# Performance work log

Hardware: AMD Instinct MI355X
Metric: run time of the kernel (lower is better)

The kernel has to match this reference:

```python
import jax, jax.numpy as jnp
import numpy as np

EMBED_DIM = 1024
NUM_HEADS = 16
HEAD_DIM = EMBED_DIM // NUM_HEADS
ROPE_BASE = 10000.0


def _rope_cos_sin(seq_len, head_dim, dtype):
    # Standard RoPE (ESM-style rotate_half): freqs outer(t, inv_freq), emb = cat(freqs, freqs)
    inv_freq = 1.0 / (ROPE_BASE ** (jnp.arange(0, head_dim, 2, dtype=jnp.float32) / head_dim))
    t = jnp.arange(seq_len, dtype=jnp.float32)
    freqs = jnp.einsum('s,d->sd', t, inv_freq)          # [s, d/2]
    emb = jnp.concatenate([freqs, freqs], axis=-1)      # [s, d]
    return jnp.cos(emb).astype(dtype), jnp.sin(emb).astype(dtype)


def _rotate_half(x):
    x1, x2 = jnp.split(x, 2, axis=-1)
    return jnp.concatenate([-x2, x1], axis=-1)


def _apply_rope(x, cos, sin):
    # x: [b, h, s, d]; cos/sin: [s, d] broadcast over b, h
    return x * cos + _rotate_half(x) * sin


def setup_inputs() -> dict:
    key = jax.random.key(0)
    ks = jax.random.split(key, 5)
    b, s, e = 4, 2048, EMBED_DIM
    scale = 1.0 / np.sqrt(e)
    x = jax.random.normal(ks[0], (b, s, e), dtype=jnp.float32)
    Wqkv = jax.random.normal(ks[1], (e, 3 * e), dtype=jnp.float32) * scale
    bqkv = jnp.zeros((3 * e,), dtype=jnp.float32)
    Wo = jax.random.normal(ks[2], (e, e), dtype=jnp.float32) * scale
    bo = jnp.zeros((e,), dtype=jnp.float32)
    return {"x": x, "Wqkv": Wqkv, "bqkv": bqkv, "Wo": Wo, "bo": bo}


def reference(x, Wqkv, bqkv, Wo, bo):
    b, s, e = x.shape
    h, d = NUM_HEADS, HEAD_DIM
    qkv = jnp.einsum('bse,ef->bsf', x, Wqkv) + bqkv          # [b, s, 3e]
    q, k, v = jnp.split(qkv, 3, axis=-1)
    # b s (h d) -> b h s d
    q = q.reshape(b, s, h, d).transpose(0, 2, 1, 3)
    k = k.reshape(b, s, h, d).transpose(0, 2, 1, 3)
    v = v.reshape(b, s, h, d).transpose(0, 2, 1, 3)
    cos, sin = _rope_cos_sin(s, d, x.dtype)
    q = _apply_rope(q, cos, sin)
    k = _apply_rope(k, cos, sin)
    # scaled dot product attention (no mask, no dropout, non-causal)
    scores = jnp.einsum('bhqd,bhkd->bhqk', q, k) / jnp.asarray(np.sqrt(d), x.dtype)
    attn = jax.nn.softmax(scores, axis=-1)
    out = jnp.einsum('bhqk,bhkd->bhqd', attn, v)             # [b, h, s, d]
    out = out.transpose(0, 2, 1, 3).reshape(b, s, e)         # b h s d -> b s (h d)
    return jnp.einsum('bse,ef->bsf', out, Wo) + bo
```

## Files before the change

### kernel.cpp

```cpp
#include <hip/hip_runtime.h>
#include <stdint.h>
#include <stddef.h>

typedef __bf16 bf16;
typedef __attribute__((ext_vector_type(8))) __bf16 bf16x8;
typedef __attribute__((ext_vector_type(4))) __bf16 bf16x4;
typedef __attribute__((ext_vector_type(4))) float f32x4;
typedef __attribute__((ext_vector_type(4))) float float4v;

#define BATCH 4
#define SEQ   2048
#define EMB   1024
#define NH    16
#define HD    64
#define F3    3072

#define MFMA16(a, b, c) __builtin_amdgcn_mfma_f32_16x16x32_bf16((a), (b), (c), 0, 0, 0)

__device__ __forceinline__ void gload_lds16(const bf16* g, bf16* l) {
  __builtin_amdgcn_global_load_lds(
      (const __attribute__((address_space(1))) uint32_t*)g,
      (__attribute__((address_space(3))) uint32_t*)l, 16, 0, 0);
}

__device__ __forceinline__ int mod10(int x) { return x >= 10 ? x - 10 : x; }

__global__ __launch_bounds__(256) void rope_table(float* __restrict__ cosT,
                                                  float* __restrict__ sinT) {
  int idx = blockIdx.x * 256 + threadIdx.x;
  int pos = idx >> 5, d1 = idx & 31;
  float inv = powf(10000.0f, -(float)(2 * d1) / 64.0f);
  float th = (float)pos * inv;
  cosT[idx] = cosf(th);
  sinT[idx] = sinf(th);
}

__global__ __launch_bounds__(256) void convert_bf16(const float* __restrict__ src,
                                                    bf16* __restrict__ dst, int n4) {
  int i = blockIdx.x * 256 + threadIdx.x;
  if (i >= n4) return;
  float4v v = ((const float4v*)src)[i];
  bf16x4 o;
#pragma unroll
  for (int k = 0; k < 4; ++k) o[k] = (bf16)v[k];
  ((bf16x4*)dst)[i] = o;
}

__global__ __launch_bounds__(256) void transpose_f32_bf16(const float* __restrict__ in,
                                                          bf16* __restrict__ out,
                                                          int R, int C) {
  __shared__ bf16 tile[32][33];
  const int tx = threadIdx.x & 31;
  const int ty = threadIdx.x >> 5;
  const int c0 = blockIdx.x * 32, r0 = blockIdx.y * 32;
#pragma unroll
  for (int kk = 0; kk < 4; ++kk) {
    int r = ty + kk * 8;
    tile[r][tx] = (bf16)in[(size_t)(r0 + r) * C + c0 + tx];
  }
  __syncthreads();
#pragma unroll
  for (int kk = 0; kk < 4; ++kk) {
    int r = ty + kk * 8;
    out[(size_t)(c0 + r) * R + r0 + tx] = tile[tx][r];
  }
}

__device__ __forceinline__ void gemm256_core(bf16* lds,
                                             const bf16* __restrict__ Abase,
                                             const bf16* __restrict__ Bbase,
                                             f32x4 (&acc)[8][4]) {
  const int tid = threadIdx.x;
  const int w = tid >> 6, lane = tid & 63;
  const int lhi = lane >> 4, llo = lane & 15, l7 = llo & 7;
  const int wr = w >> 2, wc = w & 3;
  const int srow = lane >> 3;
  const int sk16 = (lane & 7) ^ srow;
  const size_t g_lane = (size_t)(w * 16 + srow) * EMB + sk16 * 8;
  bf16* ldsw = lds + w * 1024;

  const int ka0 = (lhi * 8) ^ (l7 << 3);
  const int ka1 = (32 + lhi * 8) ^ (l7 << 3);
  const int arow = llo * 64;
  const int brow = ((wc & 1) * 64 + llo) * 64;

#pragma unroll
  for (int i = 0; i < 8; ++i)
#pragma unroll
    for (int j = 0; j < 4; ++j) acc[i][j] = (f32x4){0.f, 0.f, 0.f, 0.f};

#define STAGE(baseptr, slot)                              \
  do {                                                    \
    const bf16* _b = (baseptr);                           \
    bf16* _l = ldsw + (slot) * 8192;                      \
    gload_lds16(_b + g_lane, _l);                         \
    gload_lds16(_b + g_lane + 8 * EMB, _l + 512);         \
  } while (0)

  STAGE(Abase, 0);
  STAGE(Abase + 128 * EMB, 1);
  STAGE(Bbase, 2);
  STAGE(Bbase + 128 * EMB, 3);
  STAGE(Abase + 64, 4);
  STAGE(Abase + 128 * EMB + 64, 5);
  asm volatile("s_waitcnt vmcnt(4)" ::: "memory");
  __builtin_amdgcn_s_barrier();

  int rs = 0;
#pragma unroll 1
  for (int t = 0; t < 16; ++t) {
    const bf16* ldsA = lds + mod10(rs + wr) * 8192 + arow;
    const bf16* ldsB = lds + mod10(rs + 2 + (wc >> 1)) * 8192 + brow;
    const int k1 = (t + 1) * 64;
    const int k2 = (t + 2) * 64;
    bf16x8 a[4][2], b0[2][2], b1[2][2];

#pragma unroll
    for (int i = 0; i < 4; ++i) {
      a[i][0] = *(const bf16x8*)(ldsA + i * 1024 + ka0);
      a[i][1] = *(const bf16x8*)(ldsA + i * 1024 + ka1);
    }
#pragma unroll
    for (int j = 0; j < 2; ++j) {
      b0[j][0] = *(const bf16x8*)(ldsB + j * 1024 + ka0);
      b0[j][1] = *(const bf16x8*)(ldsB + j * 1024 + ka1);
    }
    if (t < 15) STAGE(Bbase + k1, mod10(rs + 6));
    __builtin_amdgcn_s_barrier();
    asm volatile("s_waitcnt lgkmcnt(0)" ::: "memory");
    __builtin_amdgcn_sched_barrier(0);
    __builtin_amdgcn_s_setprio(1);
#pragma unroll
    for (int i = 0; i < 4; ++i)
#pragma unroll
      for (int j = 0; j < 2; ++j) {
        acc[i][j] = MFMA16(a[i][0], b0[j][0], acc[i][j]);
        acc[i][j] = MFMA16(a[i][1], b0[j][1], acc[i][j]);
      }
    __builtin_amdgcn_s_setprio(0);
    __builtin_amdgcn_s_barrier();

#pragma unroll
    for (int j = 0; j < 2; ++j) {
      b1[j][0] = *(const bf16x8*)(ldsB + 2048 + j * 1024 + ka0);
      b1[j][1] = *(const bf16x8*)(ldsB + 2048 + j * 1024 + ka1);
    }
    if (t < 15) STAGE(Bbase + 128 * EMB + k1, mod10(rs + 7));
    __builtin_amdgcn_s_barrier();
    asm volatile("s_waitcnt lgkmcnt(0)" ::: "memory");
    __builtin_amdgcn_sched_barrier(0);
    __builtin_amdgcn_s_setprio(1);
#pragma unroll
    for (int i = 0; i < 4; ++i)
#pragma unroll
      for (int j = 0; j < 2; ++j) {
        acc[i][2 + j] = MFMA16(a[i][0], b1[j][0], acc[i][2 + j]);
        acc[i][2 + j] = MFMA16(a[i][1], b1[j][1], acc[i][2 + j]);
      }
    __builtin_amdgcn_s_setprio(0);
    __builtin_amdgcn_s_barrier();

#pragma unroll
    for (int i = 0; i < 4; ++i) {
      a[i][0] = *(const bf16x8*)(ldsA + 4096 + i * 1024 + ka0);
      a[i][1] = *(const bf16x8*)(ldsA + 4096 + i * 1024 + ka1);
    }
    if (t < 14) STAGE(Abase + k2, mod10(rs + 8));
    __builtin_amdgcn_s_barrier();
    asm volatile("s_waitcnt lgkmcnt(0)" ::: "memory");
    __builtin_amdgcn_sched_barrier(0);
    __builtin_amdgcn_s_setprio(1);
#pragma unroll
    for (int i = 0; i < 4; ++i)
#pragma unroll
      for (int j = 0; j < 2; ++j) {
        acc[4 + i][2 + j] = MFMA16(a[i][0], b1[j][0], acc[4 + i][2 + j]);
        acc[4 + i][2 + j] = MFMA16(a[i][1], b1[j][1], acc[4 + i][2 + j]);
      }
    __builtin_amdgcn_s_setprio(0);
    __builtin_amdgcn_s_barrier();

    if (t < 14) STAGE(Abase + 128 * EMB + k2, mod10(rs + 9));
    __builtin_amdgcn_s_barrier();
    asm volatile("s_waitcnt lgkmcnt(0)" ::: "memory");
    __builtin_amdgcn_sched_barrier(0);
    __builtin_amdgcn_s_setprio(1);
#pragma unroll
    for (int i = 0; i < 4; ++i)
#pragma unroll
      for (int j = 0; j < 2; ++j) {
        acc[4 + i][j] = MFMA16(a[i][0], b0[j][0], acc[4 + i][j]);
        acc[4 + i][j] = MFMA16(a[i][1], b0[j][1], acc[4 + i][j]);
      }
    __builtin_amdgcn_s_setprio(0);
    if (t < 14) {
      asm volatile("s_waitcnt vmcnt(4)" ::: "memory");
    } else if (t == 14) {
      asm volatile("s_waitcnt vmcnt(0)" ::: "memory");
    }
    if (t < 15) __builtin_amdgcn_s_barrier();

    rs += 4;
    if (rs >= 10) rs -= 10;
  }
#undef STAGE
}

__global__ __launch_bounds__(512, 2) void qkv8_kernel(
    const bf16* __restrict__ x, const bf16* __restrict__ wT,
    const float* __restrict__ bias, bf16* __restrict__ qo, bf16* __restrict__ ko,
    bf16* __restrict__ vo, const float* __restrict__ cosT,
    const float* __restrict__ sinT) {
  extern __shared__ __align__(16) bf16 ldsb[];
  const int orig = blockIdx.x;
  const int wg = (orig & 7) * 48 + (orig >> 3);
  const int bx = wg % 12, by = wg / 12;
  const int row_a0 = by * 256, row_b0 = bx * 256;

  f32x4 acc[8][4];
  gemm256_core(ldsb, x + (size_t)row_a0 * EMB, wT + (size_t)row_b0 * EMB, acc);

  const int tid = threadIdx.x;
  const int w = tid >> 6, lane = tid & 63;
  const int lhi = lane >> 4, llo = lane & 15;
  const int wr = w >> 2, wc = w & 3;

  const int f0 = row_b0 + wc * 64;
  const int part = f0 >> 10;
  const int hh = (f0 & 1023) >> 6;
  const int m_base = row_a0 + wr * 128;

  float bvals[4];
#pragma unroll
  for (int j = 0; j < 4; ++j) bvals[j] = bias[f0 + j * 16 + llo];

  if (part == 2) {
#pragma unroll
    for (int mi = 0; mi < 8; ++mi) {
      int m0 = m_base + mi * 16 + lhi * 4;
      int bb = m0 >> 11, pos0 = m0 & 2047;
#pragma unroll
      for (int j = 0; j < 4; ++j) {
        int dd = j * 16 + llo;
        bf16x4 pk;
#pragma unroll
        for (int r = 0; r < 4; ++r) pk[r] = (bf16)(acc[mi][j][r] + bvals[j]);
        *(bf16x4*)(vo + ((size_t)(bb * NH + hh) * HD + dd) * SEQ + pos0) = pk;
      }
    }
  } else {
    bf16* dst = (part == 0) ? qo : ko;
    const float qs = (part == 0) ? 0.125f : 1.0f;
#pragma unroll
    for (int mi = 0; mi < 8; ++mi) {
#pragma unroll
      for (int r = 0; r < 4; ++r) {
        int m = m_base + mi * 16 + lhi * 4 + r;
        int bb = m >> 11, pos = m & 2047;
        size_t base = ((size_t)(bb * NH + hh) * SEQ + pos) * HD;
#pragma unroll
        for (int j = 0; j < 2; ++j) {
          int d1 = j * 16 + llo;
          float x1 = acc[mi][j][r] + bvals[j];
          float x2 = acc[mi][j + 2][r] + bvals[j + 2];
          float cth = cosT[pos * 32 + d1];
          float sth = sinT[pos * 32 + d1];
          dst[base + d1] = (bf16)((x1 * cth - x2 * sth) * qs);
          dst[base + d1 + 32] = (bf16)((x2 * cth + x1 * sth) * qs);
        }
      }
    }
  }
}

__global__ __launch_bounds__(512, 2) void outproj8_kernel(
    const bf16* __restrict__ a_in, const bf16* __restrict__ wT,
    const float* __restrict__ bo, float* __restrict__ out) {
  extern __shared__ __align__(16) bf16 ldsb[];
  const int orig = blockIdx.x;
  const int wg = (orig & 7) * 16 + (orig >> 3);
  const int bx = wg % 4, by = wg / 4;
  const int row_a0 = by * 256, row_b0 = bx * 256;

  f32x4 acc[8][4];
  gemm256_core(ldsb, a_in + (size_t)row_a0 * EMB, wT + (size_t)row_b0 * EMB, acc);

  const int tid = threadIdx.x;
  const int w = tid >> 6, lane = tid & 63;
  const int lhi = lane >> 4, llo = lane & 15;
  const int wr = w >> 2, wc = w & 3;

  const int col0 = row_b0 + wc * 64;
  const int m_base = row_a0 + wr * 128;
  float bvals[4];
#pragma unroll
  for (int j = 0; j < 4; ++j) bvals[j] = bo[col0 + j * 16 + llo];
#pragma unroll
  for (int mi = 0; mi < 8; ++mi) {
#pragma unroll
    for (int r = 0; r < 4; ++r) {
      int m = m_base + mi * 16 + lhi * 4 + r;
#pragma unroll
      for (int j = 0; j < 4; ++j)
        out[(size_t)m * EMB + col0 + j * 16 + llo] = acc[mi][j][r] + bvals[j];
    }
  }
}

__global__ __launch_bounds__(512) void attn_kernel(const bf16* __restrict__ q,
                                                   const bf16* __restrict__ k,
                                                   const bf16* __restrict__ vT,
                                                   bf16* __restrict__ o) {
  __shared__ __align__(16) bf16 smem[32768];
  bf16* Qs = smem;

  const int tid = threadIdx.x, w = tid >> 6, lane = tid & 63;
  const int lhi = lane >> 4, llo = lane & 15;
  const int l7 = llo & 7;
  const int bidx = blockIdx.x;
  const int vblk = (bidx & 7) * 64 + (bidx >> 3);
  const int qt = vblk & 7, bh = vblk >> 3;
  const bf16* qbase = q + (size_t)bh * SEQ * HD + qt * 256 * HD;
  const bf16* kbase = k + (size_t)bh * SEQ * HD;
  const bf16* vbase = vT + (size_t)bh * HD * SEQ;
  bf16* Pw = smem + w * 2048;

  const int rowc = lane >> 3;
  const int sw8 = (lane & 7) ^ rowc;

#pragma unroll
  for (int c = 0; c < 4; ++c) {
    int chunk = w * 4 + c;
    int row = chunk * 8 + rowc;
    gload_lds16(qbase + (size_t)row * HD + sw8 * 8, &Qs[chunk * 512]);
  }
  if (w < 4) {
#pragma unroll
    for (int c = 0; c < 2; ++c) {
      int chunk = w * 2 + c;
      int row = chunk * 8 + rowc;
      gload_lds16(kbase + (size_t)row * HD + sw8 * 8, &smem[16384 + chunk * 512]);
    }
  } else {
#pragma unroll
    for (int c = 0; c < 2; ++c) {
      int chunk = (w - 4) * 2 + c;
      int row = chunk * 8 + rowc;
      gload_lds16(vbase + (size_t)row * SEQ + sw8 * 8, &smem[24576 + chunk * 512]);
    }
  }
  __syncthreads();

  bf16x8 qf[2][2];
#pragma unroll
  for (int i = 0; i < 2; ++i)
#pragma unroll
    for (int kc = 0; kc < 2; ++kc)
      qf[i][kc] = *(const bf16x8*)&Qs[(w * 32 + i * 16 + llo) * 64 +
                                      (((kc * 4 + lhi) ^ l7) * 8)];
  __syncthreads();

  float rsum[2] = {0.f, 0.f};
  f32x4 oacc[2][4];
#pragma unroll
  for (int i = 0; i < 2; ++i)
#pragma unroll
    for (int j = 0; j < 4; ++j) oacc[i][j] = (f32x4){0.f, 0.f, 0.f, 0.f};

  for (int kb = 0; kb < 32; ++kb) {
    bf16* Kc = smem + 16384 + (kb & 1) * 4096;
    bf16* Vc = smem + 24576 + (kb & 1) * 4096;
    if (kb < 31) {
      int kpos = (kb + 1) * 64;
      if (w < 4) {
        bf16* Kn = smem + 16384 + ((kb + 1) & 1) * 4096;
#pragma unroll
        for (int c = 0; c < 2; ++c) {
          int chunk = w * 2 + c;
          int row = chunk * 8 + rowc;
          gload_lds16(kbase + (size_t)(kpos + row) * HD + sw8 * 8, &Kn[chunk * 512]);
        }
      } else {
        bf16* Vn = smem + 24576 + ((kb + 1) & 1) * 4096;
#pragma unroll
        for (int c = 0; c < 2; ++c) {
          int chunk = (w - 4) * 2 + c;
          int row = chunk * 8 + rowc;
          gload_lds16(vbase + (size_t)row * SEQ + kpos + sw8 * 8, &Vn[chunk * 512]);
        }
      }
    }
    f32x4 st[4][2];
#pragma unroll
    for (int tt = 0; tt < 4; ++tt)
#pragma unroll
      for (int i = 0; i < 2; ++i) st[tt][i] = (f32x4){0.f, 0.f, 0.f, 0.f};
#pragma unroll
    for (int kc = 0; kc < 2; ++kc) {
      bf16x8 kfr[4];
#pragma unroll
      for (int tt = 0; tt < 4; ++tt)
        kfr[tt] = *(const bf16x8*)&Kc[(tt * 16 + llo) * 64 +
                                      (((kc * 4 + lhi) ^ l7) * 8)];
#pragma unroll
      for (int tt = 0; tt < 4; ++tt)
#pragma unroll
        for (int i = 0; i < 2; ++i)
          st[tt][i] = MFMA16(kfr[tt], qf[i][kc], st[tt][i]);
    }
#pragma unroll
    for (int tt = 0; tt < 4; ++tt) {
#pragma unroll
      for (int i = 0; i < 2; ++i) {
        bf16x4 pk;
        float a = 0.f;
#pragma unroll
        for (int r = 0; r < 4; ++r) {
          float p = __expf(st[tt][i][r]);
          pk[r] = (bf16)p;
          a += p;
        }
        rsum[i] += a;
        int gi = (tt * 4 + lhi) ^ (l7 << 1);
        *(bf16x4*)&Pw[(i * 16 + llo) * 64 + gi * 4] = pk;
      }
    }
#pragma unroll
    for (int kc = 0; kc < 2; ++kc) {
      bf16x8 af[2], bv[4];
      int xg = ((kc * 4 + lhi) ^ l7) * 8;
      int pg = ((kc * 8 + lhi * 2) ^ (l7 << 1)) * 4;
#pragma unroll
      for (int i = 0; i < 2; ++i)
        af[i] = *(const bf16x8*)&Pw[(i * 16 + llo) * 64 + pg];
#pragma unroll
      for (int jd = 0; jd < 4; ++jd)
        bv[jd] = *(const bf16x8*)&Vc[(jd * 16 + llo) * 64 + xg];
#pragma unroll
      for (int i = 0; i < 2; ++i)
#pragma unroll
        for (int jd = 0; jd < 4; ++jd) oacc[i][jd] = MFMA16(af[i], bv[jd], oacc[i][jd]);
    }
    __syncthreads();
  }

  const int bb = bh >> 4, hh = bh & 15;
#pragma unroll
  for (int i = 0; i < 2; ++i) {
    float t = rsum[i];
    t += __shfl_xor(t, 16);
    t += __shfl_xor(t, 32);
#pragma unroll
    for (int r = 0; r < 4; ++r) {
      float l = __shfl(t, lhi * 4 + r);
      float inv = 1.0f / l;
      int pos = qt * 256 + w * 32 + i * 16 + lhi * 4 + r;
      size_t base = ((size_t)bb * SEQ + pos) * EMB + hh * HD;
#pragma unroll
      for (int jd = 0; jd < 4; ++jd)
        o[base + jd * 16 + llo] = (bf16)(oacc[i][jd][r] * inv);
    }
  }
}

extern "C" void kernel_launch(void* const* d_in, const int* in_sizes, int n_in,
                              void* d_out, int out_size, void* d_ws, size_t ws_size,
                              hipStream_t stream) {
  const float* x_raw = (const float*)d_in[0];
  const float* wqkv_raw = (const float*)d_in[1];
  const float* bqkv = (const float*)d_in[2];
  const float* wo_raw = (const float*)d_in[3];
  const float* bo = (const float*)d_in[4];
  float* out = (float*)d_out;

  char* ws = (char*)d_ws;
  bf16* qw = (bf16*)(ws);
  bf16* kw = (bf16*)(ws + 16777216);
  bf16* vw = (bf16*)(ws + 33554432);
  bf16* wqkvT = (bf16*)(ws + 50331648);
  float* cosT = (float*)(ws + 56623104);
  float* sinT = (float*)(ws + 56885248);
  bf16* ow = (bf16*)(ws + 50331648);
  bf16* woT = (bf16*)(ws);
  bf16* xb = (bf16*)d_out;

  static bool attr_set = false;
  if (!attr_set) {
    (void)hipFuncSetAttribute((const void*)qkv8_kernel,
                              hipFuncAttributeMaxDynamicSharedMemorySize, 163840);
    (void)hipFuncSetAttribute((const void*)outproj8_kernel,
                              hipFuncAttributeMaxDynamicSharedMemorySize, 163840);
    attr_set = true;
  }

  rope_table<<<256, 256, 0, stream>>>(cosT, sinT);
  convert_bf16<<<(BATCH * SEQ * EMB / 4 + 255) / 256, 256, 0, stream>>>(
      x_raw, xb, BATCH * SEQ * EMB / 4);
  transpose_f32_bf16<<<dim3(F3 / 32, EMB / 32), 256, 0, stream>>>(wqkv_raw, wqkvT, EMB, F3);

  qkv8_kernel<<<dim3((BATCH * SEQ / 256) * (F3 / 256)), 512, 163840, stream>>>(
      xb, wqkvT, bqkv, qw, kw, vw, cosT, sinT);
  attn_kernel<<<dim3(BATCH * NH * (SEQ / 256)), 512, 0, stream>>>(qw, kw, vw, ow);

  transpose_f32_bf16<<<dim3(EMB / 32, EMB / 32), 256, 0, stream>>>(wo_raw, woT, EMB, EMB);
  outproj8_kernel<<<dim3((BATCH * SEQ / 256) * (EMB / 256)), 512, 163840, stream>>>(
      ow, woT, bo, out);
}
```

Baseline: 290.7 us.

## Rewrite attention with 32x32 MFMA and register-resident P via permlane swap

Replaces the 16x16x32 MFMA attention kernel with one built on 32x32x16 MFMAs. The probability tile now stays in registers, using packed bf16 conversion and v_permlane32_swap instead of a round trip through LDS. Q is loaded straight into registers, which halves LDS use to 32KB, and launch bounds now ask for two blocks per CU; s_setprio hints are added around the MFMA sections. The intent is to cut LDS traffic and barriers and to raise occupancy, at the cost of heavier register pressure from the 16-wide accumulators.

```diff
diff --git a/kernel.cpp b/kernel.cpp
--- a/kernel.cpp
+++ b/kernel.cpp
@@ -6,7 +6,9 @@
 typedef __attribute__((ext_vector_type(8))) __bf16 bf16x8;
 typedef __attribute__((ext_vector_type(4))) __bf16 bf16x4;
 typedef __attribute__((ext_vector_type(4))) float f32x4;
+typedef __attribute__((ext_vector_type(16))) float f32x16;
 typedef __attribute__((ext_vector_type(4))) float float4v;
+typedef __attribute__((ext_vector_type(4))) uint32_t u32x4;
 
 #define BATCH 4
 #define SEQ   2048
@@ -16,6 +18,7 @@
 #define F3    3072
 
 #define MFMA16(a, b, c) __builtin_amdgcn_mfma_f32_16x16x32_bf16((a), (b), (c), 0, 0, 0)
+#define MFMA32(a, b, c) __builtin_amdgcn_mfma_f32_32x32x16_bf16((a), (b), (c), 0, 0, 0)
 
 __device__ __forceinline__ void gload_lds16(const bf16* g, bf16* l) {
   __builtin_amdgcn_global_load_lds(
@@ -307,159 +310,156 @@
   }
 }
 
-__global__ __launch_bounds__(512) void attn_kernel(const bf16* __restrict__ q,
-                                                   const bf16* __restrict__ k,
-                                                   const bf16* __restrict__ vT,
-                                                   bf16* __restrict__ o) {
-  __shared__ __align__(16) bf16 smem[32768];
-  bf16* Qs = smem;
+__global__ __launch_bounds__(512, 2) void attn32_kernel(const bf16* __restrict__ q,
+                                                        const bf16* __restrict__ k,
+                                                        const bf16* __restrict__ vT,
+                                                        bf16* __restrict__ o) {
+  __shared__ __align__(16) bf16 smem[16384];
 
   const int tid = threadIdx.x, w = tid >> 6, lane = tid & 63;
-  const int lhi = lane >> 4, llo = lane & 15;
-  const int l7 = llo & 7;
+  const int l31 = lane & 31, hi = lane >> 5;
   const int bidx = blockIdx.x;
   const int vblk = (bidx & 7) * 64 + (bidx >> 3);
   const int qt = vblk & 7, bh = vblk >> 3;
   const bf16* qbase = q + (size_t)bh * SEQ * HD + qt * 256 * HD;
   const bf16* kbase = k + (size_t)bh * SEQ * HD;
   const bf16* vbase = vT + (size_t)bh * HD * SEQ;
-  bf16* Pw = smem + w * 2048;
 
   const int rowc = lane >> 3;
   const int sw8 = (lane & 7) ^ rowc;
 
-#pragma unroll
-  for (int c = 0; c < 4; ++c) {
-    int chunk = w * 4 + c;
-    int row = chunk * 8 + rowc;
-    gload_lds16(qbase + (size_t)row * HD + sw8 * 8, &Qs[chunk * 512]);
-  }
+  bf16x8 qf[4];
+  {
+    const bf16* qrow = qbase + (size_t)(w * 32 + l31) * HD;
+#pragma unroll
+    for (int c = 0; c < 4; ++c) qf[c] = *(const bf16x8*)(qrow + c * 16 + hi * 8);
+  }
+
   if (w < 4) {
 #pragma unroll
     for (int c = 0; c < 2; ++c) {
-      int chunk = w * 2 + c;
-      int row = chunk * 8 + rowc;
-      gload_lds16(kbase + (size_t)row * HD + sw8 * 8, &smem[16384 + chunk * 512]);
+      int ch = w * 2 + c, row = ch * 8 + rowc;
+      gload_lds16(kbase + (size_t)row * HD + sw8 * 8, &smem[ch * 512]);
     }
   } else {
 #pragma unroll
     for (int c = 0; c < 2; ++c) {
-      int chunk = (w - 4) * 2 + c;
-      int row = chunk * 8 + rowc;
-      gload_lds16(vbase + (size_t)row * SEQ + sw8 * 8, &smem[24576 + chunk * 512]);
+      int ch = (w - 4) * 2 + c, row = ch * 8 + rowc;
+      gload_lds16(vbase + (size_t)row * SEQ + sw8 * 8, &smem[8192 + ch * 512]);
     }
   }
   __syncthreads();
 
-  bf16x8 qf[2][2];
-#pragma unroll
-  for (int i = 0; i < 2; ++i)
-#pragma unroll
-    for (int kc = 0; kc < 2; ++kc)
-      qf[i][kc] = *(const bf16x8*)&Qs[(w * 32 + i * 16 + llo) * 64 +
-                                      (((kc * 4 + lhi) ^ l7) * 8)];
-  __syncthreads();
-
-  float rsum[2] = {0.f, 0.f};
-  f32x4 oacc[2][4];
-#pragma unroll
-  for (int i = 0; i < 2; ++i)
-#pragma unroll
-    for (int j = 0; j < 4; ++j) oacc[i][j] = (f32x4){0.f, 0.f, 0.f, 0.f};
+  float rsum = 0.f;
+  f32x16 oacc[2];
+#pragma unroll
+  for (int r = 0; r < 16; ++r) { oacc[0][r] = 0.f; oacc[1][r] = 0.f; }
+
+  const int swz = (l31 & 7);
 
   for (int kb = 0; kb < 32; ++kb) {
-    bf16* Kc = smem + 16384 + (kb & 1) * 4096;
-    bf16* Vc = smem + 24576 + (kb & 1) * 4096;
+    bf16* Kc = smem + (kb & 1) * 4096;
+    bf16* Vc = smem + 8192 + (kb & 1) * 4096;
     if (kb < 31) {
       int kpos = (kb + 1) * 64;
       if (w < 4) {
-        bf16* Kn = smem + 16384 + ((kb + 1) & 1) * 4096;
+        bf16* Kn = smem + ((kb + 1) & 1) * 4096;
 #pragma unroll
         for (int c = 0; c < 2; ++c) {
-          int chunk = w * 2 + c;
-          int row = chunk * 8 + rowc;
-          gload_lds16(kbase + (size_t)(kpos + row) * HD + sw8 * 8, &Kn[chunk * 512]);
+          int ch = w * 2 + c, row = ch * 8 + rowc;
+          gload_lds16(kbase + (size_t)(kpos + row) * HD + sw8 * 8, &Kn[ch * 512]);
         }
       } else {
-        bf16* Vn = smem + 24576 + ((kb + 1) & 1) * 4096;
+        bf16* Vn = smem + 8192 + ((kb + 1) & 1) * 4096;
 #pragma unroll
         for (int c = 0; c < 2; ++c) {
-          int chunk = (w - 4) * 2 + c;
-          int row = chunk * 8 + rowc;
-          gload_lds16(vbase + (size_t)row * SEQ + kpos + sw8 * 8, &Vn[chunk * 512]);
+          int ch = (w - 4) * 2 + c, row = ch * 8 + rowc;
+          gload_lds16(vbase + (size_t)row * SEQ + kpos + sw8 * 8, &Vn[ch * 512]);
         }
       }
     }
-    f32x4 st[4][2];
-#pragma unroll
-    for (int tt = 0; tt < 4; ++tt)
-#pragma unroll
-      for (int i = 0; i < 2; ++i) st[tt][i] = (f32x4){0.f, 0.f, 0.f, 0.f};
-#pragma unroll
-    for (int kc = 0; kc < 2; ++kc) {
-      bf16x8 kfr[4];
-#pragma unroll
-      for (int tt = 0; tt < 4; ++tt)
-        kfr[tt] = *(const bf16x8*)&Kc[(tt * 16 + llo) * 64 +
-                                      (((kc * 4 + lhi) ^ l7) * 8)];
-#pragma unroll
-      for (int tt = 0; tt < 4; ++tt)
-#pragma unroll
-        for (int i = 0; i < 2; ++i)
-          st[tt][i] = MFMA16(kfr[tt], qf[i][kc], st[tt][i]);
-    }
-#pragma unroll
-    for (int tt = 0; tt < 4; ++tt) {
-#pragma unroll
-      for (int i = 0; i < 2; ++i) {
-        bf16x4 pk;
-        float a = 0.f;
-#pragma unroll
-        for (int r = 0; r < 4; ++r) {
-          float p = __expf(st[tt][i][r]);
-          pk[r] = (bf16)p;
-          a += p;
-        }
-        rsum[i] += a;
-        int gi = (tt * 4 + lhi) ^ (l7 << 1);
-        *(bf16x4*)&Pw[(i * 16 + llo) * 64 + gi * 4] = pk;
-      }
-    }
-#pragma unroll
-    for (int kc = 0; kc < 2; ++kc) {
-      bf16x8 af[2], bv[4];
-      int xg = ((kc * 4 + lhi) ^ l7) * 8;
-      int pg = ((kc * 8 + lhi * 2) ^ (l7 << 1)) * 4;
-#pragma unroll
-      for (int i = 0; i < 2; ++i)
-        af[i] = *(const bf16x8*)&Pw[(i * 16 + llo) * 64 + pg];
-#pragma unroll
-      for (int jd = 0; jd < 4; ++jd)
-        bv[jd] = *(const bf16x8*)&Vc[(jd * 16 + llo) * 64 + xg];
-#pragma unroll
-      for (int i = 0; i < 2; ++i)
-#pragma unroll
-        for (int jd = 0; jd < 4; ++jd) oacc[i][jd] = MFMA16(af[i], bv[jd], oacc[i][jd]);
-    }
+
+    f32x16 st0, st1;
+#pragma unroll
+    for (int r = 0; r < 16; ++r) { st0[r] = 0.f; st1[r] = 0.f; }
+    __builtin_amdgcn_s_setprio(1);
+#pragma unroll
+    for (int c = 0; c < 4; ++c) {
+      bf16x8 kf0 = *(const bf16x8*)&Kc[l31 * 64 + (((c * 2 + hi) ^ swz) * 8)];
+      bf16x8 kf1 = *(const bf16x8*)&Kc[(32 + l31) * 64 + (((c * 2 + hi) ^ swz) * 8)];
+      st0 = MFMA32(kf0, qf[c], st0);
+      st1 = MFMA32(kf1, qf[c], st1);
+    }
+    __builtin_amdgcn_s_setprio(0);
+
+#pragma unroll
+    for (int r = 0; r < 16; ++r) {
+      st0[r] = __expf(st0[r]);
+      st1[r] = __expf(st1[r]);
+    }
+    {
+      float a0 = 0.f, a1 = 0.f, a2 = 0.f, a3 = 0.f;
+#pragma unroll
+      for (int r = 0; r < 16; r += 4) {
+        a0 += st0[r];     a1 += st0[r + 1];
+        a2 += st0[r + 2]; a3 += st0[r + 3];
+      }
+#pragma unroll
+      for (int r = 0; r < 16; r += 4) {
+        a0 += st1[r];     a1 += st1[r + 1];
+        a2 += st1[r + 2]; a3 += st1[r + 3];
+      }
+      rsum += (a0 + a1) + (a2 + a3);
+    }
+
+    bf16x8 pa[4];
+#pragma unroll
+    for (int tt = 0; tt < 2; ++tt) {
+#pragma unroll
+      for (int c1 = 0; c1 < 2; ++c1) {
+        float s0 = tt ? st1[c1 * 8 + 0] : st0[c1 * 8 + 0];
+        float s1 = tt ? st1[c1 * 8 + 1] : st0[c1 * 8 + 1];
+        float s2 = tt ? st1[c1 * 8 + 2] : st0[c1 * 8 + 2];
+        float s3 = tt ? st1[c1 * 8 + 3] : st0[c1 * 8 + 3];
+        float s4 = tt ? st1[c1 * 8 + 4] : st0[c1 * 8 + 4];
+        float s5 = tt ? st1[c1 * 8 + 5] : st0[c1 * 8 + 5];
+        float s6 = tt ? st1[c1 * 8 + 6] : st0[c1 * 8 + 6];
+        float s7 = tt ? st1[c1 * 8 + 7] : st0[c1 * 8 + 7];
+        uint32_t a0, a1, b0, b1;
+        asm("v_cvt_pk_bf16_f32 %0, %1, %2" : "=v"(a0) : "v"(s0), "v"(s1));
+        asm("v_cvt_pk_bf16_f32 %0, %1, %2" : "=v"(a1) : "v"(s2), "v"(s3));
+        asm("v_cvt_pk_bf16_f32 %0, %1, %2" : "=v"(b0) : "v"(s4), "v"(s5));
+        asm("v_cvt_pk_bf16_f32 %0, %1, %2" : "=v"(b1) : "v"(s6), "v"(s7));
+        asm("v_permlane32_swap_b32 %0, %1" : "+v"(a0), "+v"(b0));
+        asm("v_permlane32_swap_b32 %0, %1" : "+v"(a1), "+v"(b1));
+        u32x4 uv = {a0, a1, b0, b1};
+        pa[tt * 2 + c1] = __builtin_bit_cast(bf16x8, uv);
+      }
+    }
+
+    __builtin_amdgcn_s_setprio(1);
+#pragma unroll
+    for (int c = 0; c < 4; ++c) {
+      bf16x8 v0 = *(const bf16x8*)&Vc[l31 * 64 + (((c * 2 + hi) ^ swz) * 8)];
+      bf16x8 v1 = *(const bf16x8*)&Vc[(32 + l31) * 64 + (((c * 2 + hi) ^ swz) * 8)];
+      oacc[0] = MFMA32(pa[c], v0, oacc[0]);
+      oacc[1] = MFMA32(pa[c], v1, oacc[1]);
+    }
+    __builtin_amdgcn_s_setprio(0);
+
     __syncthreads();
   }
 
+  rsum += __shfl_xor(rsum, 32);
   const int bb = bh >> 4, hh = bh & 15;
 #pragma unroll
-  for (int i = 0; i < 2; ++i) {
-    float t = rsum[i];
-    t += __shfl_xor(t, 16);
-    t += __shfl_xor(t, 32);
-#pragma unroll
-    for (int r = 0; r < 4; ++r) {
-      float l = __shfl(t, lhi * 4 + r);
-      float inv = 1.0f / l;
-      int pos = qt * 256 + w * 32 + i * 16 + lhi * 4 + r;
-      size_t base = ((size_t)bb * SEQ + pos) * EMB + hh * HD;
-#pragma unroll
-      for (int jd = 0; jd < 4; ++jd)
-        o[base + jd * 16 + llo] = (bf16)(oacc[i][jd][r] * inv);
-    }
+  for (int r = 0; r < 16; ++r) {
+    int qrow = (r & 3) + 8 * (r >> 2) + 4 * hi;
+    float inv = 1.0f / __shfl(rsum, qrow);
+    int pos = qt * 256 + w * 32 + qrow;
+    size_t base = ((size_t)bb * SEQ + pos) * EMB + hh * HD;
+    o[base + l31] = (bf16)(oacc[0][r] * inv);
+    o[base + 32 + l31] = (bf16)(oacc[1][r] * inv);
   }
 }
 
@@ -500,7 +500,7 @@
 
   qkv8_kernel<<<dim3((BATCH * SEQ / 256) * (F3 / 256)), 512, 163840, stream>>>(
       xb, wqkvT, bqkv, qw, kw, vw, cosT, sinT);
-  attn_kernel<<<dim3(BATCH * NH * (SEQ / 256)), 512, 0, stream>>>(qw, kw, vw, ow);
+  attn32_kernel<<<dim3(BATCH * NH * (SEQ / 256)), 512, 0, stream>>>(qw, kw, vw, ow);
 
   transpose_f32_bf16<<<dim3(EMB / 32, EMB / 32), 256, 0, stream>>>(wo_raw, woT, EMB, EMB);
   outproj8_kernel<<<dim3((BATCH * SEQ / 256) * (EMB / 256)), 512, 163840, stream>>>(
```

Measured after the change: 289.8 us. About the same (-0.3%).
